# Kernel tuning notes

Hardware: AMD Instinct MI355X
Metric: run time of the kernel (lower is better)

Reference implementation:

```python
import jax, jax.numpy as jnp
import numpy as np

D = 1024

def setup_inputs() -> dict:
    key = jax.random.key(0)
    ks = jax.random.split(key, 7)
    s = 1.0 / np.sqrt(D)
    x = jax.random.normal(ks[0], (8, 2048, D), dtype=jnp.float32)
    Wq = jax.random.uniform(ks[1], (D, D), jnp.float32, -s, s)
    bq = jax.random.uniform(ks[2], (D,), jnp.float32, -s, s)
    Wk = jax.random.uniform(ks[3], (D, D), jnp.float32, -s, s)
    bk = jax.random.uniform(ks[4], (D,), jnp.float32, -s, s)
    Wv = jax.random.uniform(ks[5], (D, D), jnp.float32, -s, s)
    bv = jax.random.uniform(ks[6], (D,), jnp.float32, -s, s)
    return {"x": x, "Wq": Wq, "bq": bq, "Wk": Wk, "bk": bk, "Wv": Wv, "bv": bv}

def reference(x, Wq, bq, Wk, bk, Wv, bv):
    # x: [B, N, D]; Linear weights stored [D, D] used as x @ W + b (W = torch weight.T)
    q = x @ Wq + bq
    k = x @ Wk + bk
    v = x @ Wv + bv
    scores = jnp.einsum('bnd,bmd->bnm', q, k) / jnp.sqrt(jnp.float32(x.shape[-1]))
    attn = jax.nn.softmax(scores, axis=2)
    return jnp.einsum('bnm,bmd->bnd', attn, v)
```

## Files before the change

### kernel.cpp

```cpp
#include <hip/hip_runtime.h>
#include <hip/hip_bf16.h>

typedef unsigned short u16;
typedef short bf16x8 __attribute__((ext_vector_type(8)));
typedef float f32x4 __attribute__((ext_vector_type(4)));
typedef unsigned short u16x8 __attribute__((ext_vector_type(8)));
typedef unsigned short u16x4 __attribute__((ext_vector_type(4)));

__device__ __forceinline__ u16 f2bf(float f) {
    unsigned u = __float_as_uint(f);
    return (u16)((u + 0x7FFFu + ((u >> 16) & 1u)) >> 16);
}
__device__ __forceinline__ float bf2f(u16 h) {
    return __uint_as_float(((unsigned)h) << 16);
}

__global__ __launch_bounds__(256) void cast_f32_bf16(const float4* __restrict__ src,
                                                     ushort4* __restrict__ dst, int n4) {
    int i = blockIdx.x * 256 + threadIdx.x;
    if (i < n4) {
        float4 v = src[i];
        ushort4 o;
        o.x = f2bf(v.x); o.y = f2bf(v.y); o.z = f2bf(v.z); o.w = f2bf(v.w);
        dst[i] = o;
    }
}

__global__ __launch_bounds__(256) void transpose_cast3(const float* __restrict__ W0,
                                                       const float* __restrict__ W1,
                                                       const float* __restrict__ W2,
                                                       u16* __restrict__ WT) {
    __shared__ float t[32][33];
    const float* W = (blockIdx.z == 0) ? W0 : (blockIdx.z == 1) ? W1 : W2;
    u16* Wt = WT + (long)blockIdx.z * 1048576;
    int bx = blockIdx.x * 32;
    int by = blockIdx.y * 32;
    int tx = threadIdx.x, ty = threadIdx.y;
    for (int r = ty; r < 32; r += 8)
        t[r][tx] = W[(by + r) * 1024 + bx + tx];
    __syncthreads();
    for (int r = ty; r < 32; r += 8)
        Wt[(long)(bx + r) * 1024 + by + tx] = f2bf(t[tx][r]);
}

#define GLL16(g, l)                                                     \
    __builtin_amdgcn_global_load_lds(                                   \
        (const __attribute__((address_space(1))) void*)(g),             \
        (__attribute__((address_space(3))) void*)(l), 16, 0, 0)

#define PIPE_WAIT_BAR(vmstr)                                            \
    do {                                                                \
        asm volatile("s_waitcnt " vmstr " lgkmcnt(0)" ::: "memory");    \
        __builtin_amdgcn_s_barrier();                                   \
        asm volatile("" ::: "memory");                                  \
    } while (0)

template <int MODE>
__global__ __launch_bounds__(512, 2)
void gemm_bt(const u16* __restrict__ A, int lda, long sA,
             const u16* __restrict__ Bt, int ldb, long sB,
             const float* __restrict__ bq_, const float* __restrict__ bk_,
             const float* __restrict__ bv_,
             void* __restrict__ Cout, void* __restrict__ Cout2,
             int ldc, long sC, int Kdim, float scale)
{
    __shared__ __align__(16) u16 lds[4 * 16384];

    const int tid  = threadIdx.x;
    const int wave = tid >> 6;
    const int lane = tid & 63;
    const int lrow = lane & 15;
    const int kc   = lane >> 4;

    const int gx = gridDim.x, gy = gridDim.y;
    int flat = (blockIdx.z * gy + blockIdx.y) * gx + blockIdx.x;
    int total = gx * gy * gridDim.z;
    int tile = (flat & 7) * (total >> 3) + (flat >> 3);
    const int bx = tile % gx;
    const int by = (tile / gx) % gy;
    const int bz = tile / (gx * gy);

    const u16* Ab = A + (long)bz * sA;
    const u16* Bb = Bt + (long)bz * sB;
    const int row0 = by * 256;
    const int col0 = bx * 256;
    const int wr = (wave & 1) * 128;
    const int wc = (wave >> 1) * 64;

    const int rS = tid >> 2;
    const int cS = (tid & 3) ^ ((tid >> 3) & 3);
    const u16* pa0 = Ab + (long)(row0 + rS) * lda + cS * 8;
    const u16* pa1 = pa0 + (long)128 * lda;
    const u16* pb0 = Bb + (long)(col0 + rS) * ldb + cS * 8;
    const u16* pb1 = pb0 + (long)128 * ldb;
    const int dA0 = tid * 8, dA1 = 4096 + tid * 8;
    const int dB0 = 8192 + tid * 8, dB1 = 12288 + tid * 8;

    int offA[8], offB[4];
#pragma unroll
    for (int mf = 0; mf < 8; ++mf) {
        int r = wr + mf * 16 + lrow;
        offA[mf] = r * 32 + (kc ^ ((r >> 1) & 3)) * 8;
    }
#pragma unroll
    for (int nf = 0; nf < 4; ++nf) {
        int r = wc + nf * 16 + lrow;
        offB[nf] = 8192 + r * 32 + (kc ^ ((r >> 1) & 3)) * 8;
    }

    f32x4 acc[8][4] = {};

    auto stage = [&](int t) {
        u16* lb = &lds[(t & 3) * 16384];
        int ko = t * 32;
        GLL16(pa0 + ko, lb + dA0);
        GLL16(pa1 + ko, lb + dA1);
        GLL16(pb0 + ko, lb + dB0);
        GLL16(pb1 + ko, lb + dB1);
    };

    auto compute = [&](int t) {
        const u16* lb = &lds[(t & 3) * 16384];
        bf16x8 af[8], bfr[4];
#pragma unroll
        for (int nf = 0; nf < 4; ++nf) bfr[nf] = *(const bf16x8*)&lb[offB[nf]];
#pragma unroll
        for (int mf = 0; mf < 8; ++mf) af[mf] = *(const bf16x8*)&lb[offA[mf]];
        __builtin_amdgcn_s_setprio(1);
#pragma unroll
        for (int mf = 0; mf < 8; ++mf)
#pragma unroll
            for (int nf = 0; nf < 4; ++nf)
                acc[mf][nf] = __builtin_amdgcn_mfma_f32_16x16x32_bf16(
                    af[mf], bfr[nf], acc[mf][nf], 0, 0, 0);
        __builtin_amdgcn_s_setprio(0);
    };

    const int NT = Kdim >> 5;
    stage(0); stage(1); stage(2);
    for (int t = 0; t < NT - 3; ++t) {
        PIPE_WAIT_BAR("vmcnt(8)");
        stage(t + 3);
        compute(t);
    }
    PIPE_WAIT_BAR("vmcnt(8)");
    compute(NT - 3);
    PIPE_WAIT_BAR("vmcnt(4)");
    compute(NT - 2);
    PIPE_WAIT_BAR("vmcnt(0)");
    compute(NT - 1);

    const int lq = kc;
    if (MODE == 0) {
        if (col0 < 2048) {
            const float* bp = (col0 < 1024) ? bq_ : bk_;
#pragma unroll
            for (int mf = 0; mf < 8; ++mf) {
#pragma unroll
                for (int nf = 0; nf < 4; ++nf) {
                    int col = col0 + wc + nf * 16 + lrow;
                    float badd = bp[col & 1023];
                    int rbase = row0 + wr + mf * 16 + lq * 4;
#pragma unroll
                    for (int g = 0; g < 4; ++g)
                        ((u16*)Cout)[(long)(rbase + g) * 2048 + col] =
                            f2bf(acc[mf][nf][g] + badd);
                }
            }
        } else {
#pragma unroll
            for (int mf = 0; mf < 8; ++mf) {
#pragma unroll
                for (int nf = 0; nf < 4; ++nf) {
                    int d = col0 + wc + nf * 16 + lrow - 2048;
                    float badd = bv_[d];
                    int rbase = row0 + wr + mf * 16 + lq * 4;
                    int b = rbase >> 11, m = rbase & 2047;
                    u16x4 pk;
#pragma unroll
                    for (int g = 0; g < 4; ++g) pk[g] = f2bf(acc[mf][nf][g] + badd);
                    *(u16x4*)((u16*)Cout2 + ((long)b << 21) + ((long)d << 11) + m) = pk;
                }
            }
        }
    } else {
#pragma unroll
        for (int mf = 0; mf < 8; ++mf) {
#pragma unroll
            for (int nf = 0; nf < 4; ++nf) {
                int col = col0 + wc + nf * 16 + lrow;
                int rbase = row0 + wr + mf * 16 + lq * 4;
#pragma unroll
                for (int g = 0; g < 4; ++g) {
                    long idx = (long)bz * sC + (long)(rbase + g) * ldc + col;
                    if (MODE == 2)
                        ((u16*)Cout)[idx] = f2bf(acc[mf][nf][g] * scale);
                    else
                        ((float*)Cout)[idx] = acc[mf][nf][g];
                }
            }
        }
    }
}

__global__ __launch_bounds__(256) void softmax_rows(u16* __restrict__ S) {
    __shared__ float red[4];
    const long row = blockIdx.x;
    u16* p = S + row * 2048;
    const int tid = threadIdx.x;
    const int lane = tid & 63, wv = tid >> 6;

    u16x8 raw = *(const u16x8*)(p + tid * 8);
    float v[8];
#pragma unroll
    for (int i = 0; i < 8; ++i) v[i] = bf2f(raw[i]);

    float m = -1e30f;
#pragma unroll
    for (int i = 0; i < 8; ++i) m = fmaxf(m, v[i]);
    for (int off = 32; off > 0; off >>= 1) m = fmaxf(m, __shfl_down(m, off));
    if (lane == 0) red[wv] = m;
    __syncthreads();
    m = fmaxf(fmaxf(red[0], red[1]), fmaxf(red[2], red[3]));

    float s = 0.0f;
#pragma unroll
    for (int i = 0; i < 8; ++i) { v[i] = __expf(v[i] - m); s += v[i]; }
    for (int off = 32; off > 0; off >>= 1) s += __shfl_down(s, off);
    __syncthreads();
    if (lane == 0) red[wv] = s;
    __syncthreads();
    s = red[0] + red[1] + red[2] + red[3];
    float inv = 1.0f / s;

    u16x8 o;
#pragma unroll
    for (int i = 0; i < 8; ++i) o[i] = f2bf(v[i] * inv);
    *(u16x8*)(p + tid * 8) = o;
}

extern "C" void kernel_launch(void* const* d_in, const int* in_sizes, int n_in,
                              void* d_out, int out_size, void* d_ws, size_t ws_size,
                              hipStream_t stream) {
    const float* x  = (const float*)d_in[0];
    const float* Wq = (const float*)d_in[1];
    const float* bq = (const float*)d_in[2];
    const float* Wk = (const float*)d_in[3];
    const float* bk = (const float*)d_in[4];
    const float* Wv = (const float*)d_in[5];
    const float* bv = (const float*)d_in[6];
    float* out = (float*)d_out;

    char* ws = (char*)d_ws;
    u16* xb = (u16*)(ws);
    u16* WT = (u16*)(ws + 33554432);
    u16* QK = (u16*)(ws + 39845888);
    u16* Vt = (u16*)(ws + 106954752);
    u16* S  = (u16*)(ws + 140509184);

    cast_f32_bf16<<<16384, 256, 0, stream>>>((const float4*)x, (ushort4*)xb, 4194304);
    dim3 tg(32, 32, 3), tb(32, 8);
    transpose_cast3<<<tg, tb, 0, stream>>>(Wq, Wk, Wv, WT);

    dim3 gp(12, 64, 1);
    gemm_bt<0><<<gp, 512, 0, stream>>>(xb, 1024, 0, WT, 1024, 0,
                                       bq, bk, bv, QK, Vt, 0, 0, 1024, 1.0f);

    dim3 gs(8, 8, 8);
    gemm_bt<2><<<gs, 512, 0, stream>>>(QK, 2048, 2048L * 2048, QK + 1024, 2048, 2048L * 2048,
                                       nullptr, nullptr, nullptr, S, nullptr,
                                       2048, 2048L * 2048, 1024, 0.03125f);

    softmax_rows<<<16384, 256, 0, stream>>>(S);

    dim3 gv(4, 8, 8);
    gemm_bt<3><<<gv, 512, 0, stream>>>(S, 2048, 2048L * 2048, Vt, 2048, 1024L * 2048,
                                       nullptr, nullptr, nullptr, out, nullptr,
                                       1024, 2048L * 1024, 2048, 1.0f);
}
```

Baseline: 394.4 us.

## Split each K-step into two half-phases interleaving LDS reads, loads, and MFMA

Restructures the GEMM main loop so each K tile is processed in two halves. Each half reads part of the A/B fragments from LDS and issues half of the next stage's global-to-LDS loads (A then B) before its block of MFMAs, with extra barriers between halves. The aim is to interleave memory issue with matrix math more finely, in the style of ping-pong scheduling, and to reduce register pressure from fragments. The cost is more barriers per iteration and a fragile vmcnt accounting, since loads are now split across phases.

```diff
diff --git a/kernel.cpp b/kernel.cpp
--- a/kernel.cpp
+++ b/kernel.cpp
@@ -48,13 +48,6 @@
         (const __attribute__((address_space(1))) void*)(g),             \
         (__attribute__((address_space(3))) void*)(l), 16, 0, 0)
 
-#define PIPE_WAIT_BAR(vmstr)                                            \
-    do {                                                                \
-        asm volatile("s_waitcnt " vmstr " lgkmcnt(0)" ::: "memory");    \
-        __builtin_amdgcn_s_barrier();                                   \
-        asm volatile("" ::: "memory");                                  \
-    } while (0)
-
 template <int MODE>
 __global__ __launch_bounds__(512, 2)
 void gemm_bt(const u16* __restrict__ A, int lda, long sA,
@@ -110,45 +103,72 @@
 
     f32x4 acc[8][4] = {};
 
-    auto stage = [&](int t) {
+    auto stageA = [&](int t) {
         u16* lb = &lds[(t & 3) * 16384];
         int ko = t * 32;
         GLL16(pa0 + ko, lb + dA0);
         GLL16(pa1 + ko, lb + dA1);
+    };
+    auto stageB = [&](int t) {
+        u16* lb = &lds[(t & 3) * 16384];
+        int ko = t * 32;
         GLL16(pb0 + ko, lb + dB0);
         GLL16(pb1 + ko, lb + dB1);
     };
 
-    auto compute = [&](int t) {
+    const int NT = Kdim >> 5;
+    stageA(0); stageB(0); stageA(1); stageB(1); stageA(2); stageB(2);
+    asm volatile("s_waitcnt vmcnt(8)" ::: "memory");
+    __builtin_amdgcn_s_barrier();
+
+    for (int t = 0; t < NT; ++t) {
         const u16* lb = &lds[(t & 3) * 16384];
-        bf16x8 af[8], bfr[4];
-#pragma unroll
-        for (int nf = 0; nf < 4; ++nf) bfr[nf] = *(const bf16x8*)&lb[offB[nf]];
-#pragma unroll
-        for (int mf = 0; mf < 8; ++mf) af[mf] = *(const bf16x8*)&lb[offA[mf]];
+        bf16x8 af[4], bfr[4];
+
+#pragma unroll
+        for (int i = 0; i < 4; ++i) {
+            af[i]  = *(const bf16x8*)&lb[offA[i]];
+            bfr[i] = *(const bf16x8*)&lb[offB[i]];
+        }
+        if (t + 3 < NT) stageA(t + 3);
+        __builtin_amdgcn_s_barrier();
+        asm volatile("s_waitcnt lgkmcnt(0)" ::: "memory");
         __builtin_amdgcn_s_setprio(1);
 #pragma unroll
-        for (int mf = 0; mf < 8; ++mf)
+        for (int mf = 0; mf < 4; ++mf)
 #pragma unroll
             for (int nf = 0; nf < 4; ++nf)
                 acc[mf][nf] = __builtin_amdgcn_mfma_f32_16x16x32_bf16(
                     af[mf], bfr[nf], acc[mf][nf], 0, 0, 0);
         __builtin_amdgcn_s_setprio(0);
-    };
-
-    const int NT = Kdim >> 5;
-    stage(0); stage(1); stage(2);
-    for (int t = 0; t < NT - 3; ++t) {
-        PIPE_WAIT_BAR("vmcnt(8)");
-        stage(t + 3);
-        compute(t);
-    }
-    PIPE_WAIT_BAR("vmcnt(8)");
-    compute(NT - 3);
-    PIPE_WAIT_BAR("vmcnt(4)");
-    compute(NT - 2);
-    PIPE_WAIT_BAR("vmcnt(0)");
-    compute(NT - 1);
+        __builtin_amdgcn_s_barrier();
+
+#pragma unroll
+        for (int i = 0; i < 4; ++i)
+            af[i] = *(const bf16x8*)&lb[offA[4 + i]];
+        if (t + 3 < NT) stageB(t + 3);
+        __builtin_amdgcn_s_barrier();
+        asm volatile("s_waitcnt lgkmcnt(0)" ::: "memory");
+        __builtin_amdgcn_s_setprio(1);
+#pragma unroll
+        for (int mf = 0; mf < 4; ++mf)
+#pragma unroll
+            for (int nf = 0; nf < 4; ++nf)
+                acc[4 + mf][nf] = __builtin_amdgcn_mfma_f32_16x16x32_bf16(
+                    af[mf], bfr[nf], acc[4 + mf][nf], 0, 0, 0);
+        __builtin_amdgcn_s_setprio(0);
+
+        if (t < NT - 3) {
+            asm volatile("s_waitcnt vmcnt(8) lgkmcnt(0)" ::: "memory");
+            __builtin_amdgcn_s_barrier();
+        } else if (t == NT - 3) {
+            asm volatile("s_waitcnt vmcnt(4) lgkmcnt(0)" ::: "memory");
+            __builtin_amdgcn_s_barrier();
+        } else if (t == NT - 2) {
+            asm volatile("s_waitcnt vmcnt(0) lgkmcnt(0)" ::: "memory");
+            __builtin_amdgcn_s_barrier();
+        }
+    }
 
     const int lq = kc;
     if (MODE == 0) {
```

After: 404.0 us. +2.5%, slower.

## Restructure GEMM main loop into double-buffered 64-wide K tiles with quarter staging

Applied to the files above, without the earlier changes.

The bf16 MFMA GEMM main loop moves from a 4-stage ring of 32-wide K tiles to two 64-wide K-tile buffers. Each next-tile global-to-LDS load is split into four quarter groups, and each group is interleaved with one quarter of the MFMA work. Each step waits on vmcnt and a barrier instead of waiting for a whole tile. LDS layout and swizzle are rewritten to an 8-chunk XOR pattern. The aim is to hide load latency at finer grain and reduce barrier stalls, at the cost of more barriers per tile and a fragile wait-count and buffer-reuse schedule that drops the explicit lgkmcnt wait.

```diff
diff --git a/kernel.cpp b/kernel.cpp
--- a/kernel.cpp
+++ b/kernel.cpp
@@ -48,11 +48,10 @@
         (const __attribute__((address_space(1))) void*)(g),             \
         (__attribute__((address_space(3))) void*)(l), 16, 0, 0)
 
-#define PIPE_WAIT_BAR(vmstr)                                            \
+#define VMB(n)                                                          \
     do {                                                                \
-        asm volatile("s_waitcnt " vmstr " lgkmcnt(0)" ::: "memory");    \
+        asm volatile("s_waitcnt vmcnt(" #n ")" ::: "memory");           \
         __builtin_amdgcn_s_barrier();                                   \
-        asm volatile("" ::: "memory");                                  \
     } while (0)
 
 template <int MODE>
@@ -64,13 +63,13 @@
              void* __restrict__ Cout, void* __restrict__ Cout2,
              int ldc, long sC, int Kdim, float scale)
 {
-    __shared__ __align__(16) u16 lds[4 * 16384];
+    __shared__ __align__(16) u16 lds[2 * 32768];
 
     const int tid  = threadIdx.x;
     const int wave = tid >> 6;
     const int lane = tid & 63;
     const int lrow = lane & 15;
-    const int kc   = lane >> 4;
+    const int hi   = lane >> 4;
 
     const int gx = gridDim.x, gy = gridDim.y;
     int flat = (blockIdx.z * gy + blockIdx.y) * gx + blockIdx.x;
@@ -87,70 +86,105 @@
     const int wr = (wave & 1) * 128;
     const int wc = (wave >> 1) * 64;
 
-    const int rS = tid >> 2;
-    const int cS = (tid & 3) ^ ((tid >> 3) & 3);
-    const u16* pa0 = Ab + (long)(row0 + rS) * lda + cS * 8;
-    const u16* pa1 = pa0 + (long)128 * lda;
-    const u16* pb0 = Bb + (long)(col0 + rS) * ldb + cS * 8;
-    const u16* pb1 = pb0 + (long)128 * ldb;
-    const int dA0 = tid * 8, dA1 = 4096 + tid * 8;
-    const int dB0 = 8192 + tid * 8, dB1 = 12288 + tid * 8;
-
-    int offA[8], offB[4];
-#pragma unroll
-    for (int mf = 0; mf < 8; ++mf) {
-        int r = wr + mf * 16 + lrow;
-        offA[mf] = r * 32 + (kc ^ ((r >> 1) & 3)) * 8;
+    const int t3 = tid >> 3, s7 = tid & 7;
+    const int cS = s7 ^ (t3 & 7);
+    const u16* pa = Ab + (long)(row0 + t3) * lda + cS * 8;
+    const int rB0 = ((t3 >> 5) << 6) + (t3 & 31);
+    const int rB1 = (((t3 >> 5) + 2) << 6) + (t3 & 31);
+    const u16* pb0 = Bb + (long)(col0 + rB0) * ldb + cS * 8;
+    const u16* pb1 = Bb + (long)(col0 + rB1) * ldb + cS * 8;
+    const long a64 = (long)64 * lda, a128 = (long)128 * lda;
+    const long b32 = (long)32 * ldb;
+    const int dj0 = tid * 8, dj1 = 4096 + tid * 8;
+
+#define STAGE_G(t, g)                                                       \
+    do {                                                                    \
+        u16* buf_ = &lds[((t) & 1) * 32768];                                \
+        const long ko_ = (long)(t) * 64;                                    \
+        if ((g) == 0) {                                                     \
+            GLL16(pa + ko_, buf_ + dj0);                                    \
+            GLL16(pa + a128 + ko_, buf_ + dj1);                             \
+        } else if ((g) == 1) {                                              \
+            GLL16(pb0 + ko_, buf_ + 16384 + dj0);                           \
+            GLL16(pb1 + ko_, buf_ + 16384 + dj1);                           \
+        } else if ((g) == 2) {                                              \
+            GLL16(pb0 + b32 + ko_, buf_ + 24576 + dj0);                     \
+            GLL16(pb1 + b32 + ko_, buf_ + 24576 + dj1);                     \
+        } else {                                                            \
+            GLL16(pa + a64 + ko_, buf_ + 8192 + dj0);                       \
+            GLL16(pa + a64 + a128 + ko_, buf_ + 8192 + dj1);                \
+        }                                                                   \
+    } while (0)
+
+    const int sl8 = (hi ^ (lrow & 7)) * 8;
+    const int azb = ((wave & 1) << 12) + lrow * 64 + sl8;
+    const int bzb = 16384 + ((wave >> 1) << 11) + lrow * 64 + sl8;
+
+    f32x4 acc[8][4] = {};
+    bf16x8 af[4][2], bl[2][2], bh[2][2];
+
+#define LOAD_A(lb, half)                                                    \
+    _Pragma("unroll") for (int m = 0; m < 4; ++m)                           \
+    _Pragma("unroll") for (int k = 0; k < 2; ++k)                           \
+        af[m][k] = *(const bf16x8*)&(lb)[(azb + m * 1024 + (half) * 8192) ^ (k * 32)];
+
+#define LOAD_BL(lb)                                                         \
+    _Pragma("unroll") for (int n = 0; n < 2; ++n)                           \
+    _Pragma("unroll") for (int k = 0; k < 2; ++k)                           \
+        bl[n][k] = *(const bf16x8*)&(lb)[(bzb + n * 1024) ^ (k * 32)];
+
+#define LOAD_BH(lb)                                                         \
+    _Pragma("unroll") for (int n = 0; n < 2; ++n)                           \
+    _Pragma("unroll") for (int k = 0; k < 2; ++k)                           \
+        bh[n][k] = *(const bf16x8*)&(lb)[(bzb + 8192 + n * 1024) ^ (k * 32)];
+
+#define MMA_Q(barr, mb, nb)                                                 \
+    do {                                                                    \
+        __builtin_amdgcn_s_setprio(1);                                      \
+        _Pragma("unroll") for (int k = 0; k < 2; ++k)                       \
+        _Pragma("unroll") for (int m = 0; m < 4; ++m)                       \
+        _Pragma("unroll") for (int n = 0; n < 2; ++n)                       \
+            acc[(mb) + m][(nb) + n] = __builtin_amdgcn_mfma_f32_16x16x32_bf16( \
+                af[m][k], barr[n][k], acc[(mb) + m][(nb) + n], 0, 0, 0);    \
+        __builtin_amdgcn_s_setprio(0);                                      \
+    } while (0)
+
+    const int NT = Kdim >> 6;
+    STAGE_G(0, 0); STAGE_G(0, 1); STAGE_G(0, 2); STAGE_G(0, 3);
+
+    for (int t = 0; t < NT - 1; ++t) {
+        const u16* lb = &lds[(t & 1) * 32768];
+        STAGE_G(t + 1, 0);
+        VMB(6);
+        LOAD_A(lb, 0); LOAD_BL(lb);
+        MMA_Q(bl, 0, 0);
+        STAGE_G(t + 1, 1);
+        VMB(6);
+        LOAD_BH(lb);
+        MMA_Q(bh, 0, 2);
+        STAGE_G(t + 1, 2);
+        VMB(6);
+        LOAD_A(lb, 1);
+        MMA_Q(bl, 4, 0);
+        STAGE_G(t + 1, 3);
+        VMB(6);
+        MMA_Q(bh, 4, 2);
     }
-#pragma unroll
-    for (int nf = 0; nf < 4; ++nf) {
-        int r = wc + nf * 16 + lrow;
-        offB[nf] = 8192 + r * 32 + (kc ^ ((r >> 1) & 3)) * 8;
+    {
+        const u16* lb = &lds[((NT - 1) & 1) * 32768];
+        VMB(4);
+        LOAD_A(lb, 0); LOAD_BL(lb);
+        MMA_Q(bl, 0, 0);
+        VMB(2);
+        LOAD_BH(lb);
+        MMA_Q(bh, 0, 2);
+        VMB(0);
+        LOAD_A(lb, 1);
+        MMA_Q(bl, 4, 0);
+        MMA_Q(bh, 4, 2);
     }
 
-    f32x4 acc[8][4] = {};
-
-    auto stage = [&](int t) {
-        u16* lb = &lds[(t & 3) * 16384];
-        int ko = t * 32;
-        GLL16(pa0 + ko, lb + dA0);
-        GLL16(pa1 + ko, lb + dA1);
-        GLL16(pb0 + ko, lb + dB0);
-        GLL16(pb1 + ko, lb + dB1);
-    };
-
-    auto compute = [&](int t) {
-        const u16* lb = &lds[(t & 3) * 16384];
-        bf16x8 af[8], bfr[4];
-#pragma unroll
-        for (int nf = 0; nf < 4; ++nf) bfr[nf] = *(const bf16x8*)&lb[offB[nf]];
-#pragma unroll
-        for (int mf = 0; mf < 8; ++mf) af[mf] = *(const bf16x8*)&lb[offA[mf]];
-        __builtin_amdgcn_s_setprio(1);
-#pragma unroll
-        for (int mf = 0; mf < 8; ++mf)
-#pragma unroll
-            for (int nf = 0; nf < 4; ++nf)
-                acc[mf][nf] = __builtin_amdgcn_mfma_f32_16x16x32_bf16(
-                    af[mf], bfr[nf], acc[mf][nf], 0, 0, 0);
-        __builtin_amdgcn_s_setprio(0);
-    };
-
-    const int NT = Kdim >> 5;
-    stage(0); stage(1); stage(2);
-    for (int t = 0; t < NT - 3; ++t) {
-        PIPE_WAIT_BAR("vmcnt(8)");
-        stage(t + 3);
-        compute(t);
-    }
-    PIPE_WAIT_BAR("vmcnt(8)");
-    compute(NT - 3);
-    PIPE_WAIT_BAR("vmcnt(4)");
-    compute(NT - 2);
-    PIPE_WAIT_BAR("vmcnt(0)");
-    compute(NT - 1);
-
-    const int lq = kc;
+    const int lq = hi;
     if (MODE == 0) {
         if (col0 < 2048) {
             const float* bp = (col0 < 1024) ? bq_ : bk_;
```

Result: faster. 367.3 us (-6.9%).
